# Optimization experiments

Hardware: AMD Instinct MI355X
Metric: run time of the kernel (lower is better)

The kernel has to match this reference:

```python
import jax, jax.numpy as jnp
import numpy as np

H = 8  # num_heads in nn.MultiheadAttention


def setup_inputs() -> dict:
    key = jax.random.key(0)
    ks = jax.random.split(key, 8)
    B, S, D, M = 32, 64, 512, 8192
    query = jax.random.normal(ks[0], (B, S, D), dtype=jnp.float32)
    memory = jax.random.normal(ks[1], (B, S, D), dtype=jnp.float32)
    memory_bank = jax.random.normal(ks[2], (M, D), dtype=jnp.float32)
    # nn.MultiheadAttention params: packed in_proj (3D, D) + bias, out_proj (D, D) + bias
    in_proj_w = jax.random.normal(ks[3], (3 * D, D), dtype=jnp.float32) / np.sqrt(D)
    in_proj_b = jnp.zeros((3 * D,), dtype=jnp.float32)
    out_proj_w = jax.random.normal(ks[4], (D, D), dtype=jnp.float32) / np.sqrt(D)
    out_proj_b = jnp.zeros((D,), dtype=jnp.float32)
    return {
        "query": query,
        "memory": memory,
        "memory_bank": memory_bank,
        "in_proj_w": in_proj_w,
        "in_proj_b": in_proj_b,
        "out_proj_w": out_proj_w,
        "out_proj_b": out_proj_b,
        "ptr": 17,
    }


def _retrieve(query, memory_bank, in_proj_w, in_proj_b, out_proj_w, out_proj_b):
    B, S, D = query.shape
    M = memory_bank.shape[0]
    hd = D // H
    Wq, Wk, Wv = in_proj_w[:D], in_proj_w[D:2 * D], in_proj_w[2 * D:]
    bq, bk, bv = in_proj_b[:D], in_proj_b[D:2 * D], in_proj_b[2 * D:]
    # key/value come from memory_bank expanded over batch -> identical per batch,
    # so project once: [M, D]
    q = (query @ Wq.T + bq).reshape(B, S, H, hd)
    k = (memory_bank @ Wk.T + bk).reshape(M, H, hd)
    v = (memory_bank @ Wv.T + bv).reshape(M, H, hd)
    scale = 1.0 / np.sqrt(hd).astype(np.float32)
    scores = jnp.einsum('bshd,mhd->bhsm', q * scale, k)  # [B,H,S,M]
    attn = jax.nn.softmax(scores, axis=-1)
    out = jnp.einsum('bhsm,mhd->bshd', attn, v).reshape(B, S, D)
    return out @ out_proj_w.T + out_proj_b


def _store(memory, memory_bank, ptr):
    M, D = memory_bank.shape
    flat = memory.reshape(-1, D)  # [N, D], N < M so indices are unique
    N = flat.shape[0]
    idx = (ptr + jnp.arange(N)) % M  # vectorized circular-buffer scatter
    new_bank = memory_bank.at[idx].set(flat)
    new_ptr = (ptr + N) % M
    return new_bank, new_ptr


def reference(query, memory, memory_bank, in_proj_w, in_proj_b, out_proj_w, out_proj_b, ptr):
    retrieved = _retrieve(query, memory_bank, in_proj_w, in_proj_b, out_proj_w, out_proj_b)
    new_bank, _ = _store(memory, memory_bank, ptr)
    return retrieved, new_bank
```

## Files before the change

### kernel.cpp

```cpp
#include <hip/hip_runtime.h>


#define Dm  512
#define Mb  8192
#define BSr 2048

#define QSCALE 0.18033688011112042f

typedef float f32x4 __attribute__((ext_vector_type(4)));
typedef short bf16x4 __attribute__((ext_vector_type(4)));
typedef short bf16x8 __attribute__((ext_vector_type(8)));
typedef unsigned short u16x4 __attribute__((ext_vector_type(4)));
typedef unsigned short u16x8 __attribute__((ext_vector_type(8)));
typedef unsigned u32x4 __attribute__((ext_vector_type(4)));

#define MFMA(a, b, c) __builtin_amdgcn_mfma_f32_16x16x32_bf16((a), (b), (c), 0, 0, 0)

#if __has_builtin(__builtin_amdgcn_exp2f)
#define EXP2F(x) __builtin_amdgcn_exp2f(x)
#else
#define EXP2F(x) __expf((x)*0.6931471805599453f)
#endif

__device__ __forceinline__ unsigned short f32_bf16(float f) {
  unsigned u = __builtin_bit_cast(unsigned, f);
  u += 0x7FFFu + ((u >> 16) & 1u);
  return (unsigned short)(u >> 16);
}
__device__ __forceinline__ float bf16_f32(unsigned short h) {
  unsigned u = ((unsigned)h) << 16;
  return __builtin_bit_cast(float, u);
}
__device__ __forceinline__ unsigned pack_bf16_trunc(float a, float b) {
  return (__builtin_bit_cast(unsigned, a) >> 16) |
         (__builtin_bit_cast(unsigned, b) & 0xFFFF0000u);
}

__device__ __forceinline__ void gload16(const unsigned short* g, unsigned short* l) {
  __builtin_amdgcn_global_load_lds(
      (const __attribute__((address_space(1))) void*)g,
      (__attribute__((address_space(3))) void*)l, 16, 0, 0);
}

__global__ __launch_bounds__(256) void convert_all(
    const float* __restrict__ q, const float* __restrict__ bank,
    const float* __restrict__ Win, const float* __restrict__ bin,
    const float* __restrict__ Wout, const float* __restrict__ bout,
    unsigned short* __restrict__ q_c, unsigned short* __restrict__ bank_c,
    unsigned short* __restrict__ Win_c, unsigned short* __restrict__ bin_c,
    unsigned short* __restrict__ Wout_c, unsigned short* __restrict__ bout_c) {
  const int e = (blockIdx.x * 256 + threadIdx.x) * 4;
  const float* src; unsigned short* dst; int off; int sw;
  if (e < 1048576)      { src = q;    dst = q_c;    off = e;           sw = 1; }
  else if (e < 5242880) { src = bank; dst = bank_c; off = e - 1048576; sw = 1; }
  else if (e < 6029312) { src = Win;  dst = Win_c;  off = e - 5242880; sw = 1; }
  else if (e < 6030848) { src = bin;  dst = bin_c;  off = e - 6029312; sw = 0; }
  else if (e < 6292992) { src = Wout; dst = Wout_c; off = e - 6030848; sw = 0; }
  else                  { src = bout; dst = bout_c; off = e - 6292992; sw = 0; }
  f32x4 v = *(const f32x4*)(src + off);
  u16x4 o;
#pragma unroll
  for (int j = 0; j < 4; ++j) o[j] = f32_bf16(v[j]);
  int doff = off;
  if (sw) {
    const int row = off >> 9, col = off & 511;
    doff = (off & ~511) | ((((col >> 3) ^ (row & 7)) << 3) | (col & 7));
  }
  *(u16x4*)(dst + doff) = o;
}

__global__ __launch_bounds__(256, 2) void proj_fused(
    const unsigned short* __restrict__ q_c,
    const unsigned short* __restrict__ bank_c,
    const unsigned short* __restrict__ Win_c,
    const unsigned short* __restrict__ bin_c,
    unsigned short* __restrict__ q_s,
    unsigned short* __restrict__ k_s,
    unsigned short* __restrict__ vT_s) {
  __shared__ __align__(16) unsigned short sh[32768];
  const int lane = threadIdx.x & 63;
  const int wv   = threadIdx.x >> 6;
  const int l15  = lane & 15;
  const int qd   = lane >> 4;
  const int mh   = wv & 1;
  const int nh   = wv >> 1;

  const unsigned short *Ag, *B0, *B1;
  int h = 0, mbase, nbase = 0;
  const bool iskv = blockIdx.x < 512;
  if (iskv) {
    const int idx = blockIdx.x;
    h     = (idx >> 3) & 7;
    mbase = ((idx & 7) * 8 + (idx >> 6)) * 128;
    Ag = bank_c + mbase * Dm;
    B0 = Win_c + (Dm + h * 64) * Dm;
    B1 = Win_c + (2 * Dm + h * 64) * Dm;
  } else {
    const int idx = blockIdx.x - 512;
    mbase = (idx >> 2) * 128;
    nbase = (idx & 3) * 128;
    Ag = q_c + mbase * Dm;
    B0 = Win_c + nbase * Dm;
    B1 = Win_c + (nbase + 64) * Dm;
  }

  auto Ab = [&](int buf) { return sh + buf * 8192; };
  auto Bb = [&](int buf) { return sh + 16384 + buf * 8192; };

  auto stage = [&](int buf, int t) {
#pragma unroll
    for (int i = 0; i < 4; ++i) {
      const int chunk = i * 256 + wv * 64 + lane;
      const int row = chunk >> 3, c8 = chunk & 7;
      gload16(Ag + row * Dm + (t * 8 + c8) * 8,
              Ab(buf) + (i * 256 + wv * 64) * 8);
    }
#pragma unroll
    for (int i = 0; i < 4; ++i) {
      const int chunk = i * 256 + wv * 64 + lane;
      const int row = chunk >> 3, c8 = chunk & 7;
      const unsigned short* wb = (row < 64) ? B0 + row * Dm : B1 + (row - 64) * Dm;
      gload16(wb + (t * 8 + c8) * 8,
              Bb(buf) + (i * 256 + wv * 64) * 8);
    }
  };

  const f32x4 z4 = {0.f, 0.f, 0.f, 0.f};
  f32x4 acc[4][4];
#pragma unroll
  for (int mt = 0; mt < 4; ++mt)
#pragma unroll
    for (int nt = 0; nt < 4; ++nt) acc[mt][nt] = z4;

  auto compute = [&](int buf) {
#pragma unroll
    for (int ks = 0; ks < 2; ++ks) {
      bf16x8 af[4], bfr[4];
#pragma unroll
      for (int mt = 0; mt < 4; ++mt) {
        const int row = mh * 64 + mt * 16 + l15;
        af[mt] = *(const bf16x8*)(Ab(buf) + row * 64 + (((ks * 4 + qd) ^ (row & 7)) * 8));
      }
#pragma unroll
      for (int nt = 0; nt < 4; ++nt) {
        const int row = nh * 64 + nt * 16 + l15;
        bfr[nt] = *(const bf16x8*)(Bb(buf) + row * 64 + (((ks * 4 + qd) ^ (row & 7)) * 8));
      }
#pragma unroll
      for (int mt = 0; mt < 4; ++mt)
#pragma unroll
        for (int nt = 0; nt < 4; ++nt)
          acc[mt][nt] = MFMA(af[mt], bfr[nt], acc[mt][nt]);
    }
  };

  stage(0, 0);
  __asm__ volatile("s_waitcnt vmcnt(0)" ::: "memory");
  __syncthreads();
#pragma unroll 1
  for (int t = 0; t < 7; ++t) {
    stage((t + 1) & 1, t + 1);
    compute(t & 1);
    __asm__ volatile("s_waitcnt vmcnt(0)" ::: "memory");
    __syncthreads();
  }
  compute(1);
  __syncthreads();

  if (iskv) {
    unsigned short* Kst = sh;
    unsigned short* Vst = sh + 16384;
    if (nh == 0) {
#pragma unroll
      for (int nt = 0; nt < 4; ++nt) {
        const int d = nt * 16 + l15;
        const float bk = bf16_f32(bin_c[Dm + h * 64 + d]);
#pragma unroll
        for (int mt = 0; mt < 4; ++mt)
#pragma unroll
          for (int r = 0; r < 4; ++r) {
            const int m = mh * 64 + mt * 16 + qd * 4 + r;
            Kst[m * 72 + d] = f32_bf16(acc[mt][nt][r] + bk);
          }
      }
    } else {
#pragma unroll
      for (int nt = 0; nt < 4; ++nt) {
        const int d = nt * 16 + l15;
        const float bv = bf16_f32(bin_c[2 * Dm + h * 64 + d]);
#pragma unroll
        for (int mt = 0; mt < 4; ++mt)
#pragma unroll
          for (int r = 0; r < 4; ++r) {
            const int m = mh * 64 + mt * 16 + qd * 4 + r;
            Vst[d * 136 + m] = f32_bf16(acc[mt][nt][r] + bv);
          }
      }
    }
    __syncthreads();
#pragma unroll
    for (int p = 0; p < 4; ++p) {
      const int m  = p * 32 + (threadIdx.x >> 3);
      const int c8 = threadIdx.x & 7;
      *(u16x8*)(k_s + h * (Mb * 64) + (mbase + m) * 64 + ((c8 ^ (m & 7)) * 8)) =
          *(const u16x8*)(Kst + m * 72 + c8 * 8);
    }
#pragma unroll
    for (int p = 0; p < 4; ++p) {
      const int d    = p * 16 + (threadIdx.x >> 4);
      const int m16  = threadIdx.x & 15;
      const int base = (m16 >> 2) * 32;
      const int q4   = (m16 & 3) * 4;
      u16x4 lo = *(const u16x4*)(Vst + d * 136 + base + q4);
      u16x4 hi = *(const u16x4*)(Vst + d * 136 + base + 16 + q4);
      u16x8 o  = __builtin_shufflevector(lo, hi, 0, 1, 2, 3, 4, 5, 6, 7);
      *(u16x8*)(vT_s + (h * 64 + d) * Mb + mbase + ((m16 ^ (d & 7)) * 8)) = o;
    }
  } else {
#pragma unroll
    for (int nt = 0; nt < 4; ++nt) {
      const int n = nbase + nh * 64 + nt * 16 + l15;
      const float bf = bf16_f32(bin_c[n]);
#pragma unroll
      for (int mt = 0; mt < 4; ++mt)
#pragma unroll
        for (int r = 0; r < 4; ++r) {
          const int m = mbase + mh * 64 + mt * 16 + qd * 4 + r;
          const unsigned idx = ((unsigned)(m >> 6) * 8u + (unsigned)(n >> 6)) * 4096u +
                               (unsigned)(m & 63) * 64u + (unsigned)(n & 63);
          q_s[idx] = f32_bf16((acc[mt][nt][r] + bf) * QSCALE);
        }
    }
  }
}

__global__ __launch_bounds__(256, 2) void attn_partial(
    const unsigned short* __restrict__ q_s,
    const unsigned short* __restrict__ k_s,
    const unsigned short* __restrict__ vT_s,
    unsigned short* __restrict__ O_part,
    float* __restrict__ l_part) {
  __shared__ __align__(16) unsigned short Kbuf[2][128 * 64];
  __shared__ __align__(16) unsigned short Vbuf[2][64 * 128];

  const int lane = threadIdx.x & 63;
  const int wv   = threadIdx.x >> 6;
  const int l15  = lane & 15;
  const int qd   = lane >> 4;
  const int h    = blockIdx.x & 7;
  const int g    = blockIdx.x >> 3;
  const int part = g & 3;
  const int b    = (g >> 2) * 2 + (wv >> 1);
  const int bh   = b * 8 + h;
  const int s0   = (wv & 1) * 32;

  const unsigned short* kp = k_s  + h * (Mb * 64);
  const unsigned short* vp = vT_s + h * (Mb * 64);
  const int m0p = part * 2048;

  bf16x8 bQ[2][2];
  {
    const unsigned short* qp = q_s + bh * 4096;
#pragma unroll
    for (int sj = 0; sj < 2; ++sj)
#pragma unroll
      for (int ks = 0; ks < 2; ++ks)
        bQ[sj][ks] = *(const bf16x8*)(qp + (s0 + sj * 16 + l15) * 64 + ks * 32 + qd * 8);
  }

  const f32x4 z4 = {0.f, 0.f, 0.f, 0.f};
  f32x4 oacc[2][4];
  float lsum[2] = {0.f, 0.f};
#pragma unroll
  for (int sj = 0; sj < 2; ++sj)
#pragma unroll
    for (int dt = 0; dt < 4; ++dt) oacc[sj][dt] = z4;

  const int swz = (l15 & 7) * 8;

  auto stage = [&](int buf, int m0) {
    const unsigned short* gk = kp + (m0 + wv * 32 + (lane >> 3)) * 64 + (lane & 7) * 8;
    unsigned short* lk = &Kbuf[buf][(wv * 32) * 64];
#pragma unroll
    for (int i = 0; i < 4; ++i) gload16(gk + i * 8 * 64, lk + i * 8 * 64);
    const unsigned short* gv = vp + (wv * 16 + (lane >> 4)) * Mb + m0 + (lane & 15) * 8;
    unsigned short* lv = &Vbuf[buf][(wv * 16) * 128];
#pragma unroll
    for (int i = 0; i < 4; ++i) gload16(gv + i * 4 * Mb, lv + i * 4 * 128);
  };

  auto compute = [&](int buf) {
    const unsigned short* Kb = Kbuf[buf];
    const unsigned short* Vb = Vbuf[buf];
#pragma unroll
    for (int c2 = 0; c2 < 2; ++c2) {
      f32x4 sfr[4][2];
#pragma unroll
      for (int kt = 0; kt < 4; ++kt)
#pragma unroll
        for (int sj = 0; sj < 2; ++sj) sfr[kt][sj] = z4;
#pragma unroll
      for (int kt = 0; kt < 4; ++kt) {
        const int row = c2 * 64 + kt * 16 + l15;
#pragma unroll
        for (int ks = 0; ks < 2; ++ks) {
          bf16x8 aK = *(const bf16x8*)(Kb + row * 64 + ((ks * 32 + qd * 8) ^ swz));
#pragma unroll
          for (int sj = 0; sj < 2; ++sj)
            sfr[kt][sj] = MFMA(aK, bQ[sj][ks], sfr[kt][sj]);
        }
      }
      bf16x8 aP[2][2];
#pragma unroll
      for (int sj = 0; sj < 2; ++sj) {
#pragma unroll
        for (int c = 0; c < 2; ++c) {
          const f32x4 lo = sfr[c * 2][sj];
          const f32x4 hi = sfr[c * 2 + 1][sj];
          float e0 = EXP2F(lo[0]), e1 = EXP2F(lo[1]);
          float e2 = EXP2F(lo[2]), e3 = EXP2F(lo[3]);
          float e4 = EXP2F(hi[0]), e5 = EXP2F(hi[1]);
          float e6 = EXP2F(hi[2]), e7 = EXP2F(hi[3]);
          lsum[sj] += ((e0 + e1) + (e2 + e3)) + ((e4 + e5) + (e6 + e7));
          u32x4 pk;
          pk[0] = pack_bf16_trunc(e0, e1);
          pk[1] = pack_bf16_trunc(e2, e3);
          pk[2] = pack_bf16_trunc(e4, e5);
          pk[3] = pack_bf16_trunc(e6, e7);
          aP[sj][c] = __builtin_bit_cast(bf16x8, pk);
        }
      }
#pragma unroll
      for (int c = 0; c < 2; ++c) {
#pragma unroll
        for (int dt = 0; dt < 4; ++dt) {
          const int d = dt * 16 + l15;
          bf16x8 bV = *(const bf16x8*)(Vb + d * 128 + ((c2 * 64 + c * 32 + qd * 8) ^ swz));
#pragma unroll
          for (int sj = 0; sj < 2; ++sj)
            oacc[sj][dt] = MFMA(aP[sj][c], bV, oacc[sj][dt]);
        }
      }
    }
  };

  stage(0, m0p);
  __asm__ volatile("s_waitcnt vmcnt(0)" ::: "memory");
  __syncthreads();
#pragma unroll 1
  for (int t = 0; t < 15; ++t) {
    stage((t + 1) & 1, m0p + (t + 1) * 128);
    compute(t & 1);
    __asm__ volatile("s_waitcnt vmcnt(0)" ::: "memory");
    __syncthreads();
  }
  compute(1);

#pragma unroll
  for (int sj = 0; sj < 2; ++sj) {
    float v = lsum[sj];
    v += __shfl_xor(v, 16);
    v += __shfl_xor(v, 32);
    if (qd == 0) l_part[(bh * 4 + part) * 64 + s0 + sj * 16 + l15] = v;
  }

  unsigned short* Ob = O_part + (bh * 4 + part) * 4096;
#pragma unroll
  for (int sj = 0; sj < 2; ++sj)
#pragma unroll
    for (int dt = 0; dt < 4; ++dt)
#pragma unroll
      for (int r = 0; r < 4; ++r)
        Ob[(s0 + sj * 16 + qd * 4 + r) * 64 + dt * 16 + l15] = f32_bf16(oacc[sj][dt][r]);
}

__global__ __launch_bounds__(256) void combine_bank(
    const unsigned short* __restrict__ O_part, const float* __restrict__ l_part,
    unsigned short* __restrict__ a_stage,
    const float* __restrict__ memory, const float* __restrict__ bank,
    const int* __restrict__ ptrp, float* __restrict__ out_bank) {
  if (blockIdx.x < 1024) {
    const int e  = (blockIdx.x * 256 + threadIdx.x) * 4;
    const int bh = e >> 12;
    const int rem = e & 4095;
    const int s  = rem >> 6;
    const int d  = rem & 63;
    float acc[4] = {0.f, 0.f, 0.f, 0.f};
    float l = 0.f;
#pragma unroll
    for (int p = 0; p < 4; ++p) {
      u16x4 v = *(const u16x4*)(O_part + (bh * 4 + p) * 4096 + rem);
#pragma unroll
      for (int j = 0; j < 4; ++j) acc[j] += bf16_f32(v[j]);
      l += l_part[(bh * 4 + p) * 64 + s];
    }
    const int b = bh >> 3, h = bh & 7;
    u16x4 o;
#pragma unroll
    for (int j = 0; j < 4; ++j) o[j] = f32_bf16(acc[j] / l);
    *(u16x4*)(a_stage + (b * 64 + s) * 512 + h * 64 + d) = o;
  } else {
    const int t  = (blockIdx.x - 1024) * 256 + threadIdx.x;
    const int r  = t >> 7;
    const int c4 = (t & 127) * 4;
    const int ptr = ptrp[0];
    const unsigned off = (unsigned)(r - ptr + Mb) & (Mb - 1);
    const float* src = (off < (unsigned)BSr) ? memory + off * Dm + c4
                                             : bank + r * Dm + c4;
    *(f32x4*)(out_bank + r * Dm + c4) = *(const f32x4*)src;
  }
}

__global__ __launch_bounds__(256) void out_proj(
    const unsigned short* __restrict__ A,
    const unsigned short* __restrict__ W,
    const unsigned short* __restrict__ bias,
    float* __restrict__ out) {
  const int lane = threadIdx.x & 63;
  const int wv   = threadIdx.x >> 6;
  const int l15  = lane & 15;
  const int qd   = lane >> 4;
  const int mbase = blockIdx.y * 128 + wv * 32;
  const int nbase = blockIdx.x * 64;

  const f32x4 z4 = {0.f, 0.f, 0.f, 0.f};
  f32x4 acc[2][4];
#pragma unroll
  for (int ti = 0; ti < 2; ++ti)
#pragma unroll
    for (int j = 0; j < 4; ++j) acc[ti][j] = z4;

  const unsigned short* a0p = A + (mbase + l15) * Dm + qd * 8;
  const unsigned short* a1p = a0p + 16 * Dm;
  const unsigned short* wp  = W + (nbase + l15) * Dm + qd * 8;

#pragma unroll 4
  for (int k0 = 0; k0 < Dm; k0 += 32) {
    bf16x8 a0 = *(const bf16x8*)(a0p + k0);
    bf16x8 a1 = *(const bf16x8*)(a1p + k0);
#pragma unroll
    for (int j = 0; j < 4; ++j) {
      bf16x8 bfr = *(const bf16x8*)(wp + j * 16 * Dm + k0);
      acc[0][j] = MFMA(a0, bfr, acc[0][j]);
      acc[1][j] = MFMA(a1, bfr, acc[1][j]);
    }
  }

#pragma unroll
  for (int ti = 0; ti < 2; ++ti) {
#pragma unroll
    for (int j = 0; j < 4; ++j) {
      const int n = nbase + j * 16 + l15;
      const float bf = bf16_f32(bias[n]);
#pragma unroll
      for (int r = 0; r < 4; ++r) {
        const int m = mbase + ti * 16 + qd * 4 + r;
        out[m * Dm + n] = acc[ti][j][r] + bf;
      }
    }
  }
}

extern "C" void kernel_launch(void* const* d_in, const int* in_sizes, int n_in,
                              void* d_out, int out_size, void* d_ws, size_t ws_size,
                              hipStream_t stream) {
  const float* query = (const float*)d_in[0];
  const float* memry = (const float*)d_in[1];
  const float* bank  = (const float*)d_in[2];
  const float* Win   = (const float*)d_in[3];
  const float* bin   = (const float*)d_in[4];
  const float* Wout  = (const float*)d_in[5];
  const float* bout  = (const float*)d_in[6];
  const int*   ptrp  = (const int*)d_in[7];
  float* outf = (float*)d_out;

  char* ws = (char*)d_ws;
  unsigned short* q_c     = (unsigned short*)(ws);
  unsigned short* a_stage = (unsigned short*)(ws);
  unsigned short* bank_c  = (unsigned short*)(ws + (2u << 20));
  unsigned short* O_part  = (unsigned short*)(ws + (2u << 20));
  unsigned short* Win_c   = (unsigned short*)(ws + (10u << 20));
  unsigned short* Wout_c  = (unsigned short*)(ws + 12058624u);
  unsigned short* q_s     = (unsigned short*)(ws + (12u << 20));
  float*          l_part  = (float*)(ws + (14u << 20));
  unsigned short* bin_c   = (unsigned short*)(ws + 14942208u);
  unsigned short* bout_c  = (unsigned short*)(ws + 14945280u);

  unsigned short* kv = (unsigned short*)(outf + 1048576);
  unsigned short* k_s  = kv;
  unsigned short* vT_s = kv + 4194304;

  convert_all<<<6146, 256, 0, stream>>>(query, bank, Win, bin, Wout, bout,
                                        q_c, bank_c, Win_c, bin_c, Wout_c, bout_c);

  proj_fused<<<576, 256, 0, stream>>>(q_c, bank_c, Win_c, bin_c, q_s, k_s, vT_s);

  attn_partial<<<512, 256, 0, stream>>>(q_s, k_s, vT_s, O_part, l_part);

  combine_bank<<<5120, 256, 0, stream>>>(O_part, l_part, a_stage,
                                         memry, bank, ptrp, outf + 1048576);

  out_proj<<<dim3(8, 16), 256, 0, stream>>>(a_stage, Wout_c, bout_c, outf);
}
```

Baseline: 167.7 us.

## Split attention work across waves by key half instead of query rows

Each wave now processes all 64 query rows of its batch but only half of every 128-key tile, so K and V fragments read from LDS are reused across four query subtiles instead of two. Row sums are computed with an MFMA against a ones vector rather than scalar adds. Partial O and l from the two key-halves are then reduced through shared memory in the epilogue. This doubles the accumulator register footprint, drops the two-blocks-per-SM occupancy hint, and adds extra syncs and LDS traffic at the end of the kernel.

New measurement: 254.6 us. +51.8%, slower.

```diff
diff --git a/kernel.cpp b/kernel.cpp
--- a/kernel.cpp
+++ b/kernel.cpp
@@ -234,7 +234,7 @@
   }
 }
 
-__global__ __launch_bounds__(256, 2) void attn_partial(
+__global__ __launch_bounds__(256) void attn_partial(
     const unsigned short* __restrict__ q_s,
     const unsigned short* __restrict__ k_s,
     const unsigned short* __restrict__ vT_s,
@@ -243,38 +243,44 @@
   __shared__ __align__(16) unsigned short Kbuf[2][128 * 64];
   __shared__ __align__(16) unsigned short Vbuf[2][64 * 128];
 
-  const int lane = threadIdx.x & 63;
-  const int wv   = threadIdx.x >> 6;
-  const int l15  = lane & 15;
-  const int qd   = lane >> 4;
-  const int h    = blockIdx.x & 7;
-  const int g    = blockIdx.x >> 3;
-  const int part = g & 3;
-  const int b    = (g >> 2) * 2 + (wv >> 1);
-  const int bh   = b * 8 + h;
-  const int s0   = (wv & 1) * 32;
+  const int lane  = threadIdx.x & 63;
+  const int wv    = threadIdx.x >> 6;
+  const int l15   = lane & 15;
+  const int qd    = lane >> 4;
+  const int h     = blockIdx.x & 7;
+  const int g     = blockIdx.x >> 3;
+  const int part  = g & 3;
+  const int bpair = g >> 2;
+  const int bsel  = wv >> 1;
+  const int kh    = (wv & 1) * 64;
+  const int bh    = (bpair * 2 + bsel) * 8 + h;
 
   const unsigned short* kp = k_s  + h * (Mb * 64);
   const unsigned short* vp = vT_s + h * (Mb * 64);
   const int m0p = part * 2048;
 
-  bf16x8 bQ[2][2];
+  bf16x8 bQ[4][2];
   {
     const unsigned short* qp = q_s + bh * 4096;
 #pragma unroll
-    for (int sj = 0; sj < 2; ++sj)
+    for (int sj = 0; sj < 4; ++sj)
 #pragma unroll
       for (int ks = 0; ks < 2; ++ks)
-        bQ[sj][ks] = *(const bf16x8*)(qp + (s0 + sj * 16 + l15) * 64 + ks * 32 + qd * 8);
+        bQ[sj][ks] = *(const bf16x8*)(qp + (sj * 16 + l15) * 64 + ks * 32 + qd * 8);
   }
 
   const f32x4 z4 = {0.f, 0.f, 0.f, 0.f};
-  f32x4 oacc[2][4];
-  float lsum[2] = {0.f, 0.f};
-#pragma unroll
-  for (int sj = 0; sj < 2; ++sj)
+  f32x4 oacc[4][4];
+  f32x4 lacc[4];
+#pragma unroll
+  for (int sj = 0; sj < 4; ++sj) {
+    lacc[sj] = z4;
 #pragma unroll
     for (int dt = 0; dt < 4; ++dt) oacc[sj][dt] = z4;
+  }
+  const short one_bf16 = (short)0x3F80;
+  const bf16x8 onesb = {one_bf16, one_bf16, one_bf16, one_bf16,
+                        one_bf16, one_bf16, one_bf16, one_bf16};
 
   const int swz = (l15 & 7) * 8;
 
@@ -293,53 +299,48 @@
     const unsigned short* Kb = Kbuf[buf];
     const unsigned short* Vb = Vbuf[buf];
 #pragma unroll
-    for (int c2 = 0; c2 < 2; ++c2) {
-      f32x4 sfr[4][2];
-#pragma unroll
-      for (int kt = 0; kt < 4; ++kt)
-#pragma unroll
-        for (int sj = 0; sj < 2; ++sj) sfr[kt][sj] = z4;
-#pragma unroll
-      for (int kt = 0; kt < 4; ++kt) {
-        const int row = c2 * 64 + kt * 16 + l15;
+    for (int c = 0; c < 2; ++c) {
+      const int base = kh + c * 32;
+      f32x4 sfr[2][4];
+#pragma unroll
+      for (int kt = 0; kt < 2; ++kt)
+#pragma unroll
+        for (int sj = 0; sj < 4; ++sj) sfr[kt][sj] = z4;
+#pragma unroll
+      for (int kt = 0; kt < 2; ++kt) {
 #pragma unroll
         for (int ks = 0; ks < 2; ++ks) {
-          bf16x8 aK = *(const bf16x8*)(Kb + row * 64 + ((ks * 32 + qd * 8) ^ swz));
-#pragma unroll
-          for (int sj = 0; sj < 2; ++sj)
+          bf16x8 aK = *(const bf16x8*)(Kb + (base + kt * 16 + l15) * 64 +
+                                       ((ks * 32 + qd * 8) ^ swz));
+#pragma unroll
+          for (int sj = 0; sj < 4; ++sj)
             sfr[kt][sj] = MFMA(aK, bQ[sj][ks], sfr[kt][sj]);
         }
       }
-      bf16x8 aP[2][2];
-#pragma unroll
-      for (int sj = 0; sj < 2; ++sj) {
-#pragma unroll
-        for (int c = 0; c < 2; ++c) {
-          const f32x4 lo = sfr[c * 2][sj];
-          const f32x4 hi = sfr[c * 2 + 1][sj];
-          float e0 = EXP2F(lo[0]), e1 = EXP2F(lo[1]);
-          float e2 = EXP2F(lo[2]), e3 = EXP2F(lo[3]);
-          float e4 = EXP2F(hi[0]), e5 = EXP2F(hi[1]);
-          float e6 = EXP2F(hi[2]), e7 = EXP2F(hi[3]);
-          lsum[sj] += ((e0 + e1) + (e2 + e3)) + ((e4 + e5) + (e6 + e7));
-          u32x4 pk;
-          pk[0] = pack_bf16_trunc(e0, e1);
-          pk[1] = pack_bf16_trunc(e2, e3);
-          pk[2] = pack_bf16_trunc(e4, e5);
-          pk[3] = pack_bf16_trunc(e6, e7);
-          aP[sj][c] = __builtin_bit_cast(bf16x8, pk);
-        }
-      }
-#pragma unroll
-      for (int c = 0; c < 2; ++c) {
-#pragma unroll
-        for (int dt = 0; dt < 4; ++dt) {
-          const int d = dt * 16 + l15;
-          bf16x8 bV = *(const bf16x8*)(Vb + d * 128 + ((c2 * 64 + c * 32 + qd * 8) ^ swz));
-#pragma unroll
-          for (int sj = 0; sj < 2; ++sj)
-            oacc[sj][dt] = MFMA(aP[sj][c], bV, oacc[sj][dt]);
-        }
+      bf16x8 aP[4];
+#pragma unroll
+      for (int sj = 0; sj < 4; ++sj) {
+        float e0 = EXP2F(sfr[0][sj][0]), e1 = EXP2F(sfr[0][sj][1]);
+        float e2 = EXP2F(sfr[0][sj][2]), e3 = EXP2F(sfr[0][sj][3]);
+        float e4 = EXP2F(sfr[1][sj][0]), e5 = EXP2F(sfr[1][sj][1]);
+        float e6 = EXP2F(sfr[1][sj][2]), e7 = EXP2F(sfr[1][sj][3]);
+        u32x4 pk;
+        pk[0] = pack_bf16_trunc(e0, e1);
+        pk[1] = pack_bf16_trunc(e2, e3);
+        pk[2] = pack_bf16_trunc(e4, e5);
+        pk[3] = pack_bf16_trunc(e6, e7);
+        aP[sj] = __builtin_bit_cast(bf16x8, pk);
+      }
+#pragma unroll
+      for (int sj = 0; sj < 4; ++sj)
+        lacc[sj] = MFMA(aP[sj], onesb, lacc[sj]);
+#pragma unroll
+      for (int dt = 0; dt < 4; ++dt) {
+        bf16x8 bV = *(const bf16x8*)(Vb + (dt * 16 + l15) * 128 +
+                                     ((base + qd * 8) ^ swz));
+#pragma unroll
+        for (int sj = 0; sj < 4; ++sj)
+          oacc[sj][dt] = MFMA(aP[sj], bV, oacc[sj][dt]);
       }
     }
   };
@@ -356,22 +357,49 @@
   }
   compute(1);
 
-#pragma unroll
-  for (int sj = 0; sj < 2; ++sj) {
-    float v = lsum[sj];
-    v += __shfl_xor(v, 16);
-    v += __shfl_xor(v, 32);
-    if (qd == 0) l_part[(bh * 4 + part) * 64 + s0 + sj * 16 + l15] = v;
-  }
-
-  unsigned short* Ob = O_part + (bh * 4 + part) * 4096;
-#pragma unroll
-  for (int sj = 0; sj < 2; ++sj)
+  float* red  = (float*)&Kbuf[0][0];
+  float* lred = (float*)&Vbuf[0][0];
+
+  if (l15 == 0) {
+#pragma unroll
+    for (int sj = 0; sj < 4; ++sj)
+#pragma unroll
+      for (int r = 0; r < 4; ++r)
+        lred[wv * 64 + sj * 16 + qd * 4 + r] = lacc[sj][r];
+  }
+  __syncthreads();
+  if (threadIdx.x < 128) {
+    const int s  = threadIdx.x & 63;
+    const int bs = threadIdx.x >> 6;
+    l_part[(((bpair * 2 + bs) * 8 + h) * 4 + part) * 64 + s] =
+        lred[bs * 128 + s] + lred[bs * 128 + 64 + s];
+  }
+
+  unsigned short* Ob0 = O_part + (((bpair * 2 + 0) * 8 + h) * 4 + part) * 4096;
+  unsigned short* Ob1 = O_part + (((bpair * 2 + 1) * 8 + h) * 4 + part) * 4096;
+#pragma unroll 1
+  for (int sj = 0; sj < 4; ++sj) {
+    __syncthreads();
 #pragma unroll
     for (int dt = 0; dt < 4; ++dt)
 #pragma unroll
       for (int r = 0; r < 4; ++r)
-        Ob[(s0 + sj * 16 + qd * 4 + r) * 64 + dt * 16 + l15] = f32_bf16(oacc[sj][dt][r]);
+        red[wv * 1024 + dt * 256 + r * 64 + lane] = oacc[sj][dt][r];
+    __syncthreads();
+#pragma unroll
+    for (int j = 0; j < 4; ++j) {
+      const int idx = j * 256 + threadIdx.x;
+      const float v0 = red[idx] + red[1024 + idx];
+      const float v1 = red[2048 + idx] + red[3072 + idx];
+      const int ln = idx & 63;
+      const int r  = (idx >> 6) & 3;
+      const int dt = idx >> 8;
+      const int srow = sj * 16 + (ln >> 4) * 4 + r;
+      const int dcol = dt * 16 + (ln & 15);
+      Ob0[srow * 64 + dcol] = f32_bf16(v0);
+      Ob1[srow * 64 + dcol] = f32_bf16(v1);
+    }
+  }
 }
 
 __global__ __launch_bounds__(256) void combine_bank(
```

## Tile out_proj through LDS with double-buffered async loads and swizzled layouts

Applied to the files above, without the earlier changes.

Rewrites the output projection GEMM to stage 128x128 tiles of A and W into shared memory using async global-to-LDS loads with double buffering, instead of each wave reading fragments directly from global memory. The producers of A (combine kernel) and W (convert kernel) now write an XOR-swizzled layout so LDS fragment reads avoid bank conflicts. The grid shrinks from 128 blocks to 64, which cuts global reload traffic but leaves fewer blocks to fill the GPU.

After: 160.0 us, median of 2. -4.6%, faster.

```diff
diff --git a/kernel.cpp b/kernel.cpp
--- a/kernel.cpp
+++ b/kernel.cpp
@@ -55,7 +55,7 @@
   else if (e < 5242880) { src = bank; dst = bank_c; off = e - 1048576; sw = 1; }
   else if (e < 6029312) { src = Win;  dst = Win_c;  off = e - 5242880; sw = 1; }
   else if (e < 6030848) { src = bin;  dst = bin_c;  off = e - 6029312; sw = 0; }
-  else if (e < 6292992) { src = Wout; dst = Wout_c; off = e - 6030848; sw = 0; }
+  else if (e < 6292992) { src = Wout; dst = Wout_c; off = e - 6030848; sw = 1; }
   else                  { src = bout; dst = bout_c; off = e - 6292992; sw = 0; }
   f32x4 v = *(const f32x4*)(src + off);
   u16x4 o;
@@ -398,7 +398,10 @@
     u16x4 o;
 #pragma unroll
     for (int j = 0; j < 4; ++j) o[j] = f32_bf16(acc[j] / l);
-    *(u16x4*)(a_stage + (b * 64 + s) * 512 + h * 64 + d) = o;
+    const int row = b * 64 + s;
+    const int col = h * 64 + d;
+    const int scol = (((col >> 3) ^ (row & 7)) << 3) | (col & 7);
+    *(u16x4*)(a_stage + row * 512 + scol) = o;
   } else {
     const int t  = (blockIdx.x - 1024) * 256 + threadIdx.x;
     const int r  = t >> 7;
@@ -411,53 +414,98 @@
   }
 }
 
-__global__ __launch_bounds__(256) void out_proj(
+__global__ __launch_bounds__(256, 2) void out_proj(
     const unsigned short* __restrict__ A,
     const unsigned short* __restrict__ W,
     const unsigned short* __restrict__ bias,
     float* __restrict__ out) {
+  __shared__ __align__(16) unsigned short sh[32768];
   const int lane = threadIdx.x & 63;
   const int wv   = threadIdx.x >> 6;
   const int l15  = lane & 15;
   const int qd   = lane >> 4;
-  const int mbase = blockIdx.y * 128 + wv * 32;
-  const int nbase = blockIdx.x * 64;
+  const int mh   = wv & 1;
+  const int nh   = wv >> 1;
+
+  const int mbase = (blockIdx.x >> 2) * 128;
+  const int nbase = (blockIdx.x & 3) * 128;
+  const unsigned short* Ag = A + mbase * Dm;
+  const unsigned short* B0 = W + nbase * Dm;
+  const unsigned short* B1 = W + (nbase + 64) * Dm;
+
+  auto Ab = [&](int buf) { return sh + buf * 8192; };
+  auto Bb = [&](int buf) { return sh + 16384 + buf * 8192; };
+
+  auto stage = [&](int buf, int t) {
+#pragma unroll
+    for (int i = 0; i < 4; ++i) {
+      const int chunk = i * 256 + wv * 64 + lane;
+      const int row = chunk >> 3, c8 = chunk & 7;
+      gload16(Ag + row * Dm + (t * 8 + c8) * 8,
+              Ab(buf) + (i * 256 + wv * 64) * 8);
+    }
+#pragma unroll
+    for (int i = 0; i < 4; ++i) {
+      const int chunk = i * 256 + wv * 64 + lane;
+      const int row = chunk >> 3, c8 = chunk & 7;
+      const unsigned short* wb = (row < 64) ? B0 + row * Dm : B1 + (row - 64) * Dm;
+      gload16(wb + (t * 8 + c8) * 8,
+              Bb(buf) + (i * 256 + wv * 64) * 8);
+    }
+  };
 
   const f32x4 z4 = {0.f, 0.f, 0.f, 0.f};
-  f32x4 acc[2][4];
-#pragma unroll
-  for (int ti = 0; ti < 2; ++ti)
-#pragma unroll
-    for (int j = 0; j < 4; ++j) acc[ti][j] = z4;
-
-  const unsigned short* a0p = A + (mbase + l15) * Dm + qd * 8;
-  const unsigned short* a1p = a0p + 16 * Dm;
-  const unsigned short* wp  = W + (nbase + l15) * Dm + qd * 8;
-
-#pragma unroll 4
-  for (int k0 = 0; k0 < Dm; k0 += 32) {
-    bf16x8 a0 = *(const bf16x8*)(a0p + k0);
-    bf16x8 a1 = *(const bf16x8*)(a1p + k0);
-#pragma unroll
-    for (int j = 0; j < 4; ++j) {
-      bf16x8 bfr = *(const bf16x8*)(wp + j * 16 * Dm + k0);
-      acc[0][j] = MFMA(a0, bfr, acc[0][j]);
-      acc[1][j] = MFMA(a1, bfr, acc[1][j]);
-    }
-  }
-
-#pragma unroll
-  for (int ti = 0; ti < 2; ++ti) {
-#pragma unroll
-    for (int j = 0; j < 4; ++j) {
-      const int n = nbase + j * 16 + l15;
-      const float bf = bf16_f32(bias[n]);
+  f32x4 acc[4][4];
+#pragma unroll
+  for (int mt = 0; mt < 4; ++mt)
+#pragma unroll
+    for (int nt = 0; nt < 4; ++nt) acc[mt][nt] = z4;
+
+  auto compute = [&](int buf) {
+#pragma unroll
+    for (int ks = 0; ks < 2; ++ks) {
+      bf16x8 af[4], bfr[4];
+#pragma unroll
+      for (int mt = 0; mt < 4; ++mt) {
+        const int row = mh * 64 + mt * 16 + l15;
+        af[mt] = *(const bf16x8*)(Ab(buf) + row * 64 + (((ks * 4 + qd) ^ (row & 7)) * 8));
+      }
+#pragma unroll
+      for (int nt = 0; nt < 4; ++nt) {
+        const int row = nh * 64 + nt * 16 + l15;
+        bfr[nt] = *(const bf16x8*)(Bb(buf) + row * 64 + (((ks * 4 + qd) ^ (row & 7)) * 8));
+      }
+#pragma unroll
+      for (int mt = 0; mt < 4; ++mt)
+#pragma unroll
+        for (int nt = 0; nt < 4; ++nt)
+          acc[mt][nt] = MFMA(af[mt], bfr[nt], acc[mt][nt]);
+    }
+  };
+
+  stage(0, 0);
+  __asm__ volatile("s_waitcnt vmcnt(0)" ::: "memory");
+  __syncthreads();
+#pragma unroll 1
+  for (int t = 0; t < 7; ++t) {
+    stage((t + 1) & 1, t + 1);
+    compute(t & 1);
+    __asm__ volatile("s_waitcnt vmcnt(0)" ::: "memory");
+    __syncthreads();
+  }
+  compute(1);
+
+#pragma unroll
+  for (int nt = 0; nt < 4; ++nt) {
+    const int n = nbase + nh * 64 + nt * 16 + l15;
+    const float bf = bf16_f32(bias[n]);
+#pragma unroll
+    for (int mt = 0; mt < 4; ++mt)
 #pragma unroll
       for (int r = 0; r < 4; ++r) {
-        const int m = mbase + ti * 16 + qd * 4 + r;
-        out[m * Dm + n] = acc[ti][j][r] + bf;
-      }
-    }
+        const int m = mbase + mh * 64 + mt * 16 + qd * 4 + r;
+        out[m * Dm + n] = acc[mt][nt][r] + bf;
+      }
   }
 }
 
@@ -500,5 +548,5 @@
   combine_bank<<<5120, 256, 0, stream>>>(O_part, l_part, a_stage,
                                          memry, bank, ptrp, outf + 1048576);
 
-  out_proj<<<dim3(8, 16), 256, 0, stream>>>(a_stage, Wout_c, bout_c, outf);
-}
+  out_proj<<<64, 256, 0, stream>>>(a_stage, Wout_c, bout_c, outf);
+}
```
